# Optimization experiments

Hardware: AMD Instinct MI355X
Metric: run time of the kernel (lower is better)

The kernel has to match this reference:

```python
import jax, jax.numpy as jnp
import numpy as np

N_HEADS = 16
N_KV_HEADS = 4
ROPE_BASE = 10000.0


def rotate_half(x):
    d = x.shape[-1] // 2
    return jnp.concatenate((-x[..., d:], x[..., :d]), axis=-1)


def rope_cos_sin(seq_len, head_dim, dtype):
    inv_freq = 1.0 / (ROPE_BASE ** (jnp.arange(0, head_dim, 2, dtype=jnp.float32) / head_dim))
    t = jnp.arange(seq_len, dtype=jnp.float32)
    freqs = jnp.outer(t, inv_freq)            # [S, d/2]
    emb = jnp.concatenate((freqs, freqs), axis=-1)  # [S, d]
    return emb.astype(dtype), None  # placeholder; cos/sin computed by caller


def setup_inputs() -> dict:
    key = jax.random.key(0)
    ks = jax.random.split(key, 5)
    B, S, H = 1, 2048, 2048
    kv_dim = (H // N_HEADS) * N_KV_HEADS  # 512
    scale = 1.0 / np.sqrt(H)
    return {
        "hidden_states": jax.random.normal(ks[0], (B, S, H), dtype=jnp.float32),
        "Wq": jax.random.normal(ks[1], (H, H), dtype=jnp.float32) * scale,
        "Wk": jax.random.normal(ks[2], (kv_dim, H), dtype=jnp.float32) * scale,
        "Wv": jax.random.normal(ks[3], (kv_dim, H), dtype=jnp.float32) * scale,
        "Wo": jax.random.normal(ks[4], (H, H), dtype=jnp.float32) * scale,
    }


def reference(hidden_states, Wq, Wk, Wv, Wo):
    B, S, H = hidden_states.shape
    nH, nKV = N_HEADS, N_KV_HEADS
    d = H // nH
    groups = nH // nKV

    # projections (nn.Linear: y = x @ W.T)
    q = (hidden_states @ Wq.T).reshape(B, S, nH, d)   # [B,S,nH,d]
    k = (hidden_states @ Wk.T).reshape(B, S, nKV, d)  # [B,S,nKV,d]
    v = (hidden_states @ Wv.T).reshape(B, S, nKV, d)

    # RoPE
    inv_freq = 1.0 / (ROPE_BASE ** (jnp.arange(0, d, 2, dtype=jnp.float32) / d))
    freqs = jnp.outer(jnp.arange(S, dtype=jnp.float32), inv_freq)  # [S,d/2]
    emb = jnp.concatenate((freqs, freqs), axis=-1)                 # [S,d]
    cos = jnp.cos(emb)[None, :, None, :]
    sin = jnp.sin(emb)[None, :, None, :]
    q = q * cos + rotate_half(q) * sin
    k = k * cos + rotate_half(k) * sin

    # GQA: repeat_interleave kv heads over head axis
    k = jnp.repeat(k, groups, axis=2)  # [B,S,nH,d]
    v = jnp.repeat(v, groups, axis=2)

    # causal scaled dot-product attention
    scores = jnp.einsum('bqhd,bkhd->bhqk', q, k) / jnp.sqrt(jnp.asarray(d, q.dtype))
    causal = jnp.tril(jnp.ones((S, S), dtype=bool))
    scores = jnp.where(causal[None, None], scores, jnp.asarray(-jnp.inf, scores.dtype))
    probs = jax.nn.softmax(scores, axis=-1)
    out = jnp.einsum('bhqk,bkhd->bqhd', probs, v)  # [B,S,nH,d]
    out = out.reshape(B, S, H) @ Wo.T
    return out
```

## Files before the change

kernel.cpp:

```cpp
#include <hip/hip_runtime.h>
#include <cstdint>
#include <cstddef>


typedef __bf16 bf16_t;
typedef bf16_t bf16x4_t __attribute__((ext_vector_type(4)));
typedef bf16_t bf16x8_t __attribute__((ext_vector_type(8)));
typedef float f32x4_t __attribute__((ext_vector_type(4)));

__device__ __forceinline__ void async_copy16(void* lds_base, const void* gsrc) {
  auto g = reinterpret_cast<__attribute__((address_space(1))) void*>(
      reinterpret_cast<uintptr_t>(gsrc));
  auto l = reinterpret_cast<__attribute__((address_space(3))) void*>(
      static_cast<uint32_t>(reinterpret_cast<uintptr_t>(lds_base)));
  __builtin_amdgcn_global_load_lds(g, l, 16, 0, 0);
}

__global__ __launch_bounds__(256) void cvt_all(const float* __restrict__ hs,
                                               const float* __restrict__ wq,
                                               const float* __restrict__ wk,
                                               const float* __restrict__ wv,
                                               bf16_t* __restrict__ regA,
                                               bf16_t* __restrict__ regB) {
  const int b = blockIdx.x;
  const float* src;
  bf16_t* dst;
  int rel;
  if (b < 4096) { src = hs; dst = regA; rel = b; }
  else if (b < 8192) { src = wq; dst = regB; rel = b - 4096; }
  else if (b < 9216) { src = wk; dst = regB + 4194304; rel = b - 8192; }
  else { src = wv; dst = regB + 5242880; rel = b - 9216; }
  const int i = (rel * 256 + threadIdx.x) * 4;
  float4 v = *(const float4*)(src + i);
  bf16x4_t o = {(bf16_t)v.x, (bf16_t)v.y, (bf16_t)v.z, (bf16_t)v.w};
  *(bf16x4_t*)(dst + i) = o;
}

__global__ __launch_bounds__(256) void cvt_bf16(const float* __restrict__ in,
                                                bf16_t* __restrict__ out, int n) {
  int i = (blockIdx.x * 256 + threadIdx.x) * 4;
  if (i >= n) return;
  float4 v = *(const float4*)(in + i);
  bf16x4_t o = {(bf16_t)v.x, (bf16_t)v.y, (bf16_t)v.z, (bf16_t)v.w};
  *(bf16x4_t*)(out + i) = o;
}

template <typename OutT, bool ROPE>
__global__ __launch_bounds__(256) void gemm_bt64(const bf16_t* __restrict__ A,
                                                 const bf16_t* __restrict__ B,
                                                 OutT* __restrict__ C,
                                                 int M, int N, int K) {
  __shared__ bf16_t As[64 * 64];
  __shared__ bf16_t Bs[128 * 64];
  const int tid = threadIdx.x;
  const int lane = tid & 63;
  const int quad = lane >> 4;
  const int l15 = lane & 15;
  const int wave = tid >> 6;
  const int bm = blockIdx.x * 64;
  const int bn = blockIdx.y * 128;
  const int wm = (wave >> 1) * 32;
  const int wn32 = (wave & 1) * 32;
  const int coff[4] = {wn32, wn32 + 16, wn32 + 64, wn32 + 80};

  f32x4_t acc[2][4] = {};

  for (int k0 = 0; k0 < K; k0 += 64) {
#pragma unroll
    for (int it = 0; it < 2; ++it) {
      const int off = it * 2048 + tid * 8;
      const int r = off >> 6;
      const int c = off & 63;
      const int wbase = it * 2048 + (tid & 192) * 8;
      async_copy16(As + wbase, A + (size_t)(bm + r) * K + k0 + c);
    }
#pragma unroll
    for (int it = 0; it < 4; ++it) {
      const int off = it * 2048 + tid * 8;
      const int r = off >> 6;
      const int c = off & 63;
      const int wbase = it * 2048 + (tid & 192) * 8;
      async_copy16(Bs + wbase, B + (size_t)(bn + r) * K + k0 + c);
    }
    __syncthreads();
#pragma unroll
    for (int kk = 0; kk < 64; kk += 32) {
      bf16x8_t af[2], bfv[4];
#pragma unroll
      for (int i = 0; i < 2; ++i)
        af[i] = *(const bf16x8_t*)(As + (wm + i * 16 + l15) * 64 + kk + quad * 8);
#pragma unroll
      for (int i = 0; i < 4; ++i)
        bfv[i] = *(const bf16x8_t*)(Bs + (coff[i] + l15) * 64 + kk + quad * 8);
#pragma unroll
      for (int mi = 0; mi < 2; ++mi)
#pragma unroll
        for (int ni = 0; ni < 4; ++ni)
          acc[mi][ni] = __builtin_amdgcn_mfma_f32_16x16x32_bf16(
              af[mi], bfv[ni], acc[mi][ni], 0, 0, 0);
    }
    __syncthreads();
  }

  if (ROPE && bn < 2560) {
#pragma unroll
    for (int pair = 0; pair < 2; ++pair) {
      const int i_d = wn32 + pair * 16 + l15;
      const float inv = exp2f(-(float)i_d * 0.20762050593045702f);
#pragma unroll
      for (int mi = 0; mi < 2; ++mi) {
#pragma unroll
        for (int r = 0; r < 4; ++r) {
          const int s_row = bm + wm + mi * 16 + quad * 4 + r;
          float sn, cs;
          sincosf((float)s_row * inv, &sn, &cs);
          const float x0 = acc[mi][pair][r];
          const float x1 = acc[mi][pair + 2][r];
          acc[mi][pair][r] = x0 * cs - x1 * sn;
          acc[mi][pair + 2][r] = x1 * cs + x0 * sn;
        }
      }
    }
  }

#pragma unroll
  for (int mi = 0; mi < 2; ++mi) {
#pragma unroll
    for (int r = 0; r < 4; ++r) {
      const int row = bm + wm + mi * 16 + quad * 4 + r;
#pragma unroll
      for (int ni = 0; ni < 4; ++ni)
        C[(size_t)row * N + bn + coff[ni] + l15] = (OutT)acc[mi][ni][r];
    }
  }
}

__global__ __launch_bounds__(256) void attn_kernel(const bf16_t* __restrict__ qkv,
                                                   bf16_t* __restrict__ out) {
  __shared__ bf16_t Ks[64 * 136];
  __shared__ bf16_t Vt[128 * 72];
  __shared__ bf16_t Ps[4 * 16 * 72];
  const int tid = threadIdx.x;
  const int lane = tid & 63;
  const int wave = tid >> 6;
  const int quad = lane >> 4;
  const int l15 = lane & 15;
  const int j = blockIdx.x;
  const int qb = (j < 256) ? (31 - (j >> 4)) : ((j - 256) >> 4);
  const int h = j & 15;
  const int kvh = h >> 2;
  const float scale = 0.08838834764831845f;

  const int rk0 = tid >> 4;
  const int ck = (tid * 8) & 127;
  const int dv2 = lane * 2;

  bf16x8_t qf[4];
  {
    const bf16_t* qbase =
        qkv + (size_t)(qb * 64 + wave * 16 + l15) * 3072 + h * 128 + quad * 8;
#pragma unroll
    for (int kf = 0; kf < 4; ++kf) qf[kf] = *(const bf16x8_t*)(qbase + kf * 32);
  }

  f32x4_t o[8] = {};
  float lsum[4] = {0.f, 0.f, 0.f, 0.f};

  bf16x8_t kreg[4];
  uint32_t vbuf[2][8];
  auto load_tile = [&](int kb) {
    const bf16_t* kbase = qkv + (size_t)(kb * 64) * 3072 + 2048 + kvh * 128;
    const bf16_t* vbase = qkv + (size_t)(kb * 64) * 3072 + 2560 + kvh * 128;
#pragma unroll
    for (int it = 0; it < 4; ++it)
      kreg[it] = *(const bf16x8_t*)(kbase + (size_t)(it * 16 + rk0) * 3072 + ck);
#pragma unroll
    for (int it = 0; it < 2; ++it) {
      const int kg8 = it * 4 + wave;
#pragma unroll
      for (int j2 = 0; j2 < 8; ++j2)
        vbuf[it][j2] =
            *(const uint32_t*)(vbase + (size_t)(kg8 * 8 + j2) * 3072 + dv2);
    }
  };

  load_tile(0);

  for (int kb = 0; kb <= qb; ++kb) {
    __syncthreads();
#pragma unroll
    for (int it = 0; it < 4; ++it)
      *(bf16x8_t*)(Ks + (it * 16 + rk0) * 136 + ck) = kreg[it];
#pragma unroll
    for (int it = 0; it < 2; ++it) {
      const int kg8 = it * 4 + wave;
      bf16x8_t lov, hiv;
#pragma unroll
      for (int j2 = 0; j2 < 8; ++j2) {
        const uint32_t u = vbuf[it][j2];
        lov[j2] = __builtin_bit_cast(bf16_t, (unsigned short)(u & 0xffff));
        hiv[j2] = __builtin_bit_cast(bf16_t, (unsigned short)(u >> 16));
      }
      *(bf16x8_t*)(Vt + (size_t)dv2 * 72 + kg8 * 8) = lov;
      *(bf16x8_t*)(Vt + (size_t)(dv2 + 1) * 72 + kg8 * 8) = hiv;
    }
    __syncthreads();
    if (kb < qb) load_tile(kb + 1);

    f32x4_t sc[4] = {};
#pragma unroll
    for (int kf = 0; kf < 4; ++kf) {
#pragma unroll
      for (int ni = 0; ni < 4; ++ni) {
        bf16x8_t bfr =
            *(const bf16x8_t*)(Ks + (ni * 16 + l15) * 136 + kf * 32 + quad * 8);
        sc[ni] = __builtin_amdgcn_mfma_f32_16x16x32_bf16(qf[kf], bfr, sc[ni], 0, 0, 0);
      }
    }

    float p[4][4];
#pragma unroll
    for (int r = 0; r < 4; ++r) {
      const int sq = qb * 64 + wave * 16 + quad * 4 + r;
#pragma unroll
      for (int ni = 0; ni < 4; ++ni) {
        float arg = fmaf(sc[ni][r], scale, -16.0f);
        if (kb == qb && (kb * 64 + ni * 16 + l15) > sq) arg = -100.0f;
        const float e = __expf(arg);
        p[ni][r] = e;
        lsum[r] += e;
      }
    }

    bf16_t* pw = Ps + wave * 16 * 72;
#pragma unroll
    for (int ni = 0; ni < 4; ++ni)
#pragma unroll
      for (int r = 0; r < 4; ++r)
        pw[(quad * 4 + r) * 72 + ni * 16 + l15] = (bf16_t)p[ni][r];

#pragma unroll
    for (int kf = 0; kf < 2; ++kf) {
      bf16x8_t af = *(const bf16x8_t*)(pw + l15 * 72 + kf * 32 + quad * 8);
#pragma unroll
      for (int ni = 0; ni < 8; ++ni) {
        bf16x8_t bfr =
            *(const bf16x8_t*)(Vt + (ni * 16 + l15) * 72 + kf * 32 + quad * 8);
        o[ni] = __builtin_amdgcn_mfma_f32_16x16x32_bf16(af, bfr, o[ni], 0, 0, 0);
      }
    }
  }

#pragma unroll
  for (int m = 1; m <= 8; m <<= 1)
#pragma unroll
    for (int r = 0; r < 4; ++r) lsum[r] += __shfl_xor(lsum[r], m, 64);

  bf16_t* obase =
      out + (size_t)(qb * 64 + wave * 16 + quad * 4) * 2048 + h * 128 + l15;
#pragma unroll
  for (int r = 0; r < 4; ++r) {
    const float inv = 1.0f / lsum[r];
#pragma unroll
    for (int ni = 0; ni < 8; ++ni)
      obase[(size_t)r * 2048 + ni * 16] = (bf16_t)(o[ni][r] * inv);
  }
}

extern "C" void kernel_launch(void* const* d_in, const int* in_sizes, int n_in,
                              void* d_out, int out_size, void* d_ws, size_t ws_size,
                              hipStream_t stream) {
  const float* hidden = (const float*)d_in[0];
  const float* Wq = (const float*)d_in[1];
  const float* Wk = (const float*)d_in[2];
  const float* Wv = (const float*)d_in[3];
  const float* Wo = (const float*)d_in[4];

  char* ws = (char*)d_ws;
  bf16_t* regA = (bf16_t*)ws;
  bf16_t* regB = (bf16_t*)(ws + (size_t)(8u << 20));
  bf16_t* regC = (bf16_t*)(ws + (size_t)(20u << 20));

  cvt_all<<<10240, 256, 0, stream>>>(hidden, Wq, Wk, Wv, regA, regB);

  gemm_bt64<bf16_t, true><<<dim3(32, 24), 256, 0, stream>>>(regA, regB, regC,
                                                            2048, 3072, 2048);

  cvt_bf16<<<4096, 256, 0, stream>>>(Wo, regA, 4194304);

  attn_kernel<<<512, 256, 0, stream>>>(regC, regB);

  gemm_bt64<float, false><<<dim3(32, 16), 256, 0, stream>>>(
      regB, regA, (float*)d_out, 2048, 2048, 2048);
}
```

Baseline: 237.3 us.

## Split attention KV range across two blocks, swizzle LDS, fuse Wo conversion

Each (query block, head) pair of the attention kernel is now split into two halves over the KV range, which doubles the grid to 1024 blocks. Each half writes unnormalized fp32 partial outputs and row sums, and a new combine kernel adds them and normalizes. The change also replaces padded LDS layouts with XOR swizzles in both the GEMM and attention kernels to avoid bank conflicts, and folds the Wo conversion into the single conversion kernel. In exchange it adds an extra launch and fp32 partial-output traffic.

```diff
diff --git a/kernel.cpp b/kernel.cpp
--- a/kernel.cpp
+++ b/kernel.cpp
@@ -20,8 +20,10 @@
                                                const float* __restrict__ wq,
                                                const float* __restrict__ wk,
                                                const float* __restrict__ wv,
+                                               const float* __restrict__ wo,
                                                bf16_t* __restrict__ regA,
-                                               bf16_t* __restrict__ regB) {
+                                               bf16_t* __restrict__ regB,
+                                               bf16_t* __restrict__ regWo) {
   const int b = blockIdx.x;
   const float* src;
   bf16_t* dst;
@@ -29,20 +31,12 @@
   if (b < 4096) { src = hs; dst = regA; rel = b; }
   else if (b < 8192) { src = wq; dst = regB; rel = b - 4096; }
   else if (b < 9216) { src = wk; dst = regB + 4194304; rel = b - 8192; }
-  else { src = wv; dst = regB + 5242880; rel = b - 9216; }
+  else if (b < 10240) { src = wv; dst = regB + 5242880; rel = b - 9216; }
+  else { src = wo; dst = regWo; rel = b - 10240; }
   const int i = (rel * 256 + threadIdx.x) * 4;
   float4 v = *(const float4*)(src + i);
   bf16x4_t o = {(bf16_t)v.x, (bf16_t)v.y, (bf16_t)v.z, (bf16_t)v.w};
   *(bf16x4_t*)(dst + i) = o;
-}
-
-__global__ __launch_bounds__(256) void cvt_bf16(const float* __restrict__ in,
-                                                bf16_t* __restrict__ out, int n) {
-  int i = (blockIdx.x * 256 + threadIdx.x) * 4;
-  if (i >= n) return;
-  float4 v = *(const float4*)(in + i);
-  bf16x4_t o = {(bf16_t)v.x, (bf16_t)v.y, (bf16_t)v.z, (bf16_t)v.w};
-  *(bf16x4_t*)(out + i) = o;
 }
 
 template <typename OutT, bool ROPE>
@@ -56,6 +50,7 @@
   const int lane = tid & 63;
   const int quad = lane >> 4;
   const int l15 = lane & 15;
+  const int l7 = l15 & 7;
   const int wave = tid >> 6;
   const int bm = blockIdx.x * 64;
   const int bn = blockIdx.y * 128;
@@ -68,30 +63,33 @@
   for (int k0 = 0; k0 < K; k0 += 64) {
 #pragma unroll
     for (int it = 0; it < 2; ++it) {
-      const int off = it * 2048 + tid * 8;
-      const int r = off >> 6;
-      const int c = off & 63;
+      const int slot = it * 256 + tid;
+      const int r = slot >> 3;
+      const int q = (slot & 7) ^ (r & 7);
       const int wbase = it * 2048 + (tid & 192) * 8;
-      async_copy16(As + wbase, A + (size_t)(bm + r) * K + k0 + c);
+      async_copy16(As + wbase, A + (size_t)(bm + r) * K + k0 + q * 8);
     }
 #pragma unroll
     for (int it = 0; it < 4; ++it) {
-      const int off = it * 2048 + tid * 8;
-      const int r = off >> 6;
-      const int c = off & 63;
+      const int slot = it * 256 + tid;
+      const int r = slot >> 3;
+      const int q = (slot & 7) ^ (r & 7);
       const int wbase = it * 2048 + (tid & 192) * 8;
-      async_copy16(Bs + wbase, B + (size_t)(bn + r) * K + k0 + c);
+      async_copy16(Bs + wbase, B + (size_t)(bn + r) * K + k0 + q * 8);
     }
     __syncthreads();
 #pragma unroll
     for (int kk = 0; kk < 64; kk += 32) {
+      const int kc = kk >> 3;
       bf16x8_t af[2], bfv[4];
 #pragma unroll
       for (int i = 0; i < 2; ++i)
-        af[i] = *(const bf16x8_t*)(As + (wm + i * 16 + l15) * 64 + kk + quad * 8);
+        af[i] = *(const bf16x8_t*)(As + (wm + i * 16 + l15) * 64 +
+                                   (((kc + quad) ^ l7) * 8));
 #pragma unroll
       for (int i = 0; i < 4; ++i)
-        bfv[i] = *(const bf16x8_t*)(Bs + (coff[i] + l15) * 64 + kk + quad * 8);
+        bfv[i] = *(const bf16x8_t*)(Bs + (coff[i] + l15) * 64 +
+                                    (((kc + quad) ^ l7) * 8));
 #pragma unroll
       for (int mi = 0; mi < 2; ++mi)
 #pragma unroll
@@ -135,24 +133,31 @@
   }
 }
 
-__global__ __launch_bounds__(256) void attn_kernel(const bf16_t* __restrict__ qkv,
-                                                   bf16_t* __restrict__ out) {
-  __shared__ bf16_t Ks[64 * 136];
-  __shared__ bf16_t Vt[128 * 72];
-  __shared__ bf16_t Ps[4 * 16 * 72];
+__global__ __launch_bounds__(256, 4) void attn_kernel(
+    const bf16_t* __restrict__ qkv, float* __restrict__ Op,
+    float* __restrict__ lp) {
+  __shared__ bf16_t Ks[64 * 128];
+  __shared__ bf16_t Vt[128 * 64];
+  __shared__ bf16_t Ps[4 * 16 * 64];
   const int tid = threadIdx.x;
   const int lane = tid & 63;
   const int wave = tid >> 6;
   const int quad = lane >> 4;
   const int l15 = lane & 15;
+  const int l7 = l15 & 7;
   const int j = blockIdx.x;
-  const int qb = (j < 256) ? (31 - (j >> 4)) : ((j - 256) >> 4);
-  const int h = j & 15;
+  const int half = j >> 9;
+  const int j2 = j & 511;
+  const int qb = (j2 < 256) ? (31 - (j2 >> 4)) : ((j2 - 256) >> 4);
+  const int h = j2 & 15;
   const int kvh = h >> 2;
+  const int nh0 = (qb + 2) >> 1;
+  const int kbS = half ? nh0 : 0;
+  const int kbE = half ? (qb + 1) : nh0;
   const float scale = 0.08838834764831845f;
 
   const int rk0 = tid >> 4;
-  const int ck = (tid * 8) & 127;
+  const int cq = tid & 15;
   const int dv2 = lane * 2;
 
   bf16x8_t qf[4];
@@ -173,80 +178,87 @@
     const bf16_t* vbase = qkv + (size_t)(kb * 64) * 3072 + 2560 + kvh * 128;
 #pragma unroll
     for (int it = 0; it < 4; ++it)
-      kreg[it] = *(const bf16x8_t*)(kbase + (size_t)(it * 16 + rk0) * 3072 + ck);
+      kreg[it] = *(const bf16x8_t*)(kbase + (size_t)(it * 16 + rk0) * 3072 + cq * 8);
 #pragma unroll
     for (int it = 0; it < 2; ++it) {
       const int kg8 = it * 4 + wave;
 #pragma unroll
-      for (int j2 = 0; j2 < 8; ++j2)
-        vbuf[it][j2] =
-            *(const uint32_t*)(vbase + (size_t)(kg8 * 8 + j2) * 3072 + dv2);
+      for (int t = 0; t < 8; ++t)
+        vbuf[it][t] =
+            *(const uint32_t*)(vbase + (size_t)(kg8 * 8 + t) * 3072 + dv2);
     }
   };
 
-  load_tile(0);
-
-  for (int kb = 0; kb <= qb; ++kb) {
-    __syncthreads();
-#pragma unroll
-    for (int it = 0; it < 4; ++it)
-      *(bf16x8_t*)(Ks + (it * 16 + rk0) * 136 + ck) = kreg[it];
-#pragma unroll
-    for (int it = 0; it < 2; ++it) {
-      const int kg8 = it * 4 + wave;
-      bf16x8_t lov, hiv;
-#pragma unroll
-      for (int j2 = 0; j2 < 8; ++j2) {
-        const uint32_t u = vbuf[it][j2];
-        lov[j2] = __builtin_bit_cast(bf16_t, (unsigned short)(u & 0xffff));
-        hiv[j2] = __builtin_bit_cast(bf16_t, (unsigned short)(u >> 16));
-      }
-      *(bf16x8_t*)(Vt + (size_t)dv2 * 72 + kg8 * 8) = lov;
-      *(bf16x8_t*)(Vt + (size_t)(dv2 + 1) * 72 + kg8 * 8) = hiv;
-    }
-    __syncthreads();
-    if (kb < qb) load_tile(kb + 1);
-
-    f32x4_t sc[4] = {};
-#pragma unroll
-    for (int kf = 0; kf < 4; ++kf) {
-#pragma unroll
-      for (int ni = 0; ni < 4; ++ni) {
-        bf16x8_t bfr =
-            *(const bf16x8_t*)(Ks + (ni * 16 + l15) * 136 + kf * 32 + quad * 8);
-        sc[ni] = __builtin_amdgcn_mfma_f32_16x16x32_bf16(qf[kf], bfr, sc[ni], 0, 0, 0);
-      }
-    }
-
-    float p[4][4];
-#pragma unroll
-    for (int r = 0; r < 4; ++r) {
-      const int sq = qb * 64 + wave * 16 + quad * 4 + r;
-#pragma unroll
-      for (int ni = 0; ni < 4; ++ni) {
-        float arg = fmaf(sc[ni][r], scale, -16.0f);
-        if (kb == qb && (kb * 64 + ni * 16 + l15) > sq) arg = -100.0f;
-        const float e = __expf(arg);
-        p[ni][r] = e;
-        lsum[r] += e;
-      }
-    }
-
-    bf16_t* pw = Ps + wave * 16 * 72;
-#pragma unroll
-    for (int ni = 0; ni < 4; ++ni)
-#pragma unroll
-      for (int r = 0; r < 4; ++r)
-        pw[(quad * 4 + r) * 72 + ni * 16 + l15] = (bf16_t)p[ni][r];
-
-#pragma unroll
-    for (int kf = 0; kf < 2; ++kf) {
-      bf16x8_t af = *(const bf16x8_t*)(pw + l15 * 72 + kf * 32 + quad * 8);
-#pragma unroll
-      for (int ni = 0; ni < 8; ++ni) {
-        bf16x8_t bfr =
-            *(const bf16x8_t*)(Vt + (ni * 16 + l15) * 72 + kf * 32 + quad * 8);
-        o[ni] = __builtin_amdgcn_mfma_f32_16x16x32_bf16(af, bfr, o[ni], 0, 0, 0);
+  if (kbS < kbE) {
+    load_tile(kbS);
+
+    for (int kb = kbS; kb < kbE; ++kb) {
+      __syncthreads();
+#pragma unroll
+      for (int it = 0; it < 4; ++it)
+        *(bf16x8_t*)(Ks + (it * 16 + rk0) * 128 + ((cq ^ rk0) * 8)) = kreg[it];
+#pragma unroll
+      for (int it = 0; it < 2; ++it) {
+        const int kg8 = it * 4 + wave;
+        bf16x8_t lov, hiv;
+#pragma unroll
+        for (int t = 0; t < 8; ++t) {
+          const uint32_t u = vbuf[it][t];
+          lov[t] = __builtin_bit_cast(bf16_t, (unsigned short)(u & 0xffff));
+          hiv[t] = __builtin_bit_cast(bf16_t, (unsigned short)(u >> 16));
+        }
+        *(bf16x8_t*)(Vt + (size_t)dv2 * 64 + ((kg8 ^ (dv2 & 7)) * 8)) = lov;
+        *(bf16x8_t*)(Vt + (size_t)(dv2 + 1) * 64 + ((kg8 ^ ((dv2 + 1) & 7)) * 8)) = hiv;
+      }
+      __syncthreads();
+      if (kb + 1 < kbE) load_tile(kb + 1);
+
+      f32x4_t sc[4] = {};
+#pragma unroll
+      for (int kf = 0; kf < 4; ++kf) {
+#pragma unroll
+        for (int ni = 0; ni < 4; ++ni) {
+          bf16x8_t bfr = *(const bf16x8_t*)(Ks + (ni * 16 + l15) * 128 +
+                                            (((kf * 4 + quad) ^ l15) * 8));
+          sc[ni] =
+              __builtin_amdgcn_mfma_f32_16x16x32_bf16(qf[kf], bfr, sc[ni], 0, 0, 0);
+        }
+      }
+
+      float p[4][4];
+#pragma unroll
+      for (int r = 0; r < 4; ++r) {
+        const int sq = qb * 64 + wave * 16 + quad * 4 + r;
+#pragma unroll
+        for (int ni = 0; ni < 4; ++ni) {
+          float arg = fmaf(sc[ni][r], scale, -16.0f);
+          if (kb == qb && (kb * 64 + ni * 16 + l15) > sq) arg = -100.0f;
+          const float e = __expf(arg);
+          p[ni][r] = e;
+          lsum[r] += e;
+        }
+      }
+
+      bf16_t* pw = Ps + wave * 16 * 64;
+#pragma unroll
+      for (int ni = 0; ni < 4; ++ni)
+#pragma unroll
+        for (int r = 0; r < 4; ++r) {
+          const int prow = quad * 4 + r;
+          pw[prow * 64 + (((ni * 2 + (l15 >> 3)) ^ (prow & 7)) * 8) + l7] =
+              (bf16_t)p[ni][r];
+        }
+
+#pragma unroll
+      for (int kf = 0; kf < 2; ++kf) {
+        bf16x8_t af = *(const bf16x8_t*)(pw + l15 * 64 +
+                                         (((kf * 4 + quad) ^ l7) * 8));
+#pragma unroll
+        for (int ni = 0; ni < 8; ++ni) {
+          bf16x8_t bfr = *(const bf16x8_t*)(Vt + (ni * 16 + l15) * 64 +
+                                            (((kf * 4 + quad) ^ l7) * 8));
+          o[ni] = __builtin_amdgcn_mfma_f32_16x16x32_bf16(af, bfr, o[ni], 0, 0, 0);
+        }
       }
     }
   }
@@ -256,15 +268,34 @@
 #pragma unroll
     for (int r = 0; r < 4; ++r) lsum[r] += __shfl_xor(lsum[r], m, 64);
 
-  bf16_t* obase =
-      out + (size_t)(qb * 64 + wave * 16 + quad * 4) * 2048 + h * 128 + l15;
+  float* obase = Op + (size_t)half * 4194304 +
+                 (size_t)(qb * 64 + wave * 16 + quad * 4) * 2048 + h * 128 + l15;
 #pragma unroll
   for (int r = 0; r < 4; ++r) {
-    const float inv = 1.0f / lsum[r];
 #pragma unroll
     for (int ni = 0; ni < 8; ++ni)
-      obase[(size_t)r * 2048 + ni * 16] = (bf16_t)(o[ni][r] * inv);
-  }
+      obase[(size_t)r * 2048 + ni * 16] = o[ni][r];
+    if (l15 == 0) {
+      const int row = qb * 64 + wave * 16 + quad * 4 + r;
+      lp[(half * 2048 + row) * 16 + h] = lsum[r];
+    }
+  }
+}
+
+__global__ __launch_bounds__(256) void combine_kernel(
+    const float* __restrict__ Op, const float* __restrict__ lp,
+    bf16_t* __restrict__ out) {
+  const int idx = (blockIdx.x * 256 + threadIdx.x) * 4;
+  const int s = idx >> 11;
+  const int col = idx & 2047;
+  const int h = col >> 7;
+  const float l = lp[s * 16 + h] + lp[(2048 + s) * 16 + h];
+  const float inv = 1.0f / l;
+  float4 a = *(const float4*)(Op + (size_t)s * 2048 + col);
+  float4 b = *(const float4*)(Op + 4194304 + (size_t)s * 2048 + col);
+  bf16x4_t o = {(bf16_t)((a.x + b.x) * inv), (bf16_t)((a.y + b.y) * inv),
+                (bf16_t)((a.z + b.z) * inv), (bf16_t)((a.w + b.w) * inv)};
+  *(bf16x4_t*)(out + idx) = o;
 }
 
 extern "C" void kernel_launch(void* const* d_in, const int* in_sizes, int n_in,
@@ -279,17 +310,20 @@
   char* ws = (char*)d_ws;
   bf16_t* regA = (bf16_t*)ws;
   bf16_t* regB = (bf16_t*)(ws + (size_t)(8u << 20));
-  bf16_t* regC = (bf16_t*)(ws + (size_t)(20u << 20));
-
-  cvt_all<<<10240, 256, 0, stream>>>(hidden, Wq, Wk, Wv, regA, regB);
+  float* Opart = (float*)(ws + (size_t)(8u << 20));
+  bf16_t* regC = (bf16_t*)(ws + (size_t)(40u << 20));
+  bf16_t* regWo = (bf16_t*)(ws + (size_t)(53u << 20));
+  float* lpart = (float*)(ws + (size_t)(61u << 20));
+
+  cvt_all<<<14336, 256, 0, stream>>>(hidden, Wq, Wk, Wv, Wo, regA, regB, regWo);
 
   gemm_bt64<bf16_t, true><<<dim3(32, 24), 256, 0, stream>>>(regA, regB, regC,
                                                             2048, 3072, 2048);
 
-  cvt_bf16<<<4096, 256, 0, stream>>>(Wo, regA, 4194304);
-
-  attn_kernel<<<512, 256, 0, stream>>>(regC, regB);
+  attn_kernel<<<1024, 256, 0, stream>>>(regC, Opart, lpart);
+
+  combine_kernel<<<4096, 256, 0, stream>>>(Opart, lpart, regA);
 
   gemm_bt64<float, false><<<dim3(32, 16), 256, 0, stream>>>(
-      regB, regA, (float*)d_out, 2048, 2048, 2048);
-}
+      regA, regWo, (float*)d_out, 2048, 2048, 2048);
+}
```

Result: slower. 275.1 us (+15.9%).
